# Kernel optimization log

Measured on AMD Instinct MI355X. Metric: run time of the kernel, lower is better.

## Reference

```python
import jax, jax.numpy as jnp
import numpy as np

HIDDEN = 1152
PATCH = 16
POS_SIZE = 64
B = 16
NP_ = 4096
IN_DIM = 3 * PATCH * PATCH  # 768


def setup_inputs() -> dict:
    key = jax.random.key(0)
    k1, k2, k3, k4, k5 = jax.random.split(key, 5)
    pixel_values = jax.random.normal(k1, (B, NP_, IN_DIM), dtype=jnp.float32)
    pixel_position_ids = jax.random.randint(k2, (B, NP_, 2), 0, POS_SIZE, dtype=jnp.int64)
    padding_positions = jax.random.randint(k3, (B, NP_), 0, 2) > 0
    # learned params: nn.Linear(input_dim, hidden, bias=False) weight is [hidden, in_dim]
    W = jax.random.normal(k4, (HIDDEN, IN_DIM), dtype=jnp.float32) / np.sqrt(IN_DIM)
    table = jax.random.normal(k5, (2, POS_SIZE, HIDDEN), dtype=jnp.float32)
    return {
        "pixel_values": pixel_values,
        "pixel_position_ids": pixel_position_ids,
        "padding_positions": padding_positions,
        "W": W,
        "table": table,
    }


def reference(pixel_values, pixel_position_ids, padding_positions, W, table):
    # input_proj: [B, N, in_dim] @ W.T -> [B, N, hidden]
    hidden_states = jnp.einsum("bnd,hd->bnh", pixel_values, W)
    # one_hot + matmul + sum over axis-of-2 is exactly a gather of the x-row
    # from table[0] plus the y-row from table[1]
    pos = jnp.clip(pixel_position_ids, 0, None)  # [B, N, 2]
    pe = table[0][pos[..., 0]] + table[1][pos[..., 1]]  # [B, N, hidden]
    pe = jnp.where(padding_positions[..., None], jnp.zeros_like(pe), pe)
    return hidden_states + pe
```

## Files before the change

### kernel.cpp

```cpp
#include <hip/hip_runtime.h>

#define HIDDEN 1152
#define IN_DIM 768
#define POS_SIZE 64
#define M_TOTAL (16 * 4096)

#define BM 64
#define NPASS 9
#define NSTAGE 12
#define TOTSTAGE (NPASS * NSTAGE)

typedef _Float16 f16x8 __attribute__((ext_vector_type(8)));
typedef float f32x4 __attribute__((ext_vector_type(4)));
typedef float f32x8v __attribute__((ext_vector_type(8)));

typedef __attribute__((address_space(1))) const void global_cv;
typedef __attribute__((address_space(3))) void lds_v;

__device__ __forceinline__ void async16(const void* g, void* l) {
    __builtin_amdgcn_global_load_lds((global_cv*)g, (lds_v*)l, 16, 0, 0);
}

__global__ __launch_bounds__(256) void pack_w(const float* __restrict__ W,
                                              _Float16* __restrict__ Wp) {
    unsigned tid = blockIdx.x * 256 + threadIdx.x;
    unsigned n = tid / 96u;
    unsigned kc = tid - n * 96u;
    f32x8v x = *(const f32x8v*)(W + (size_t)n * IN_DIM + kc * 8u);
    f16x8 h = __builtin_convertvector(x, f16x8);
    unsigned c = (n >> 4) * 1536u + kc * 16u + (n & 15u);
    ((f16x8*)Wp)[c] = h;
}

__global__ __launch_bounds__(512, 2) void gemm_pe(
    const float* __restrict__ A,
    const _Float16* __restrict__ Wp,
    const int* __restrict__ pos,
    const int* __restrict__ pad,
    const float* __restrict__ table,
    float* __restrict__ out) {
    __shared__ __align__(16) _Float16 sA[6144 * 8];
    __shared__ __align__(16) _Float16 sB[8 * 3 * 1024];

    const int m0 = blockIdx.x * BM;
    const int t = threadIdx.x;
    const int lane = t & 63;
    const int w = t >> 6;
    const int quad = lane >> 4;
    const int l15 = lane & 15;

    const f16x8* wp = (const f16x8*)Wp;
    _Float16* myB = &sB[w * 3072];

#pragma unroll
    for (int g = 0; g < 2; ++g)
#pragma unroll
        for (int kk = 0; kk < 2; ++kk)
            async16(wp + (size_t)(w * 1536 + (2 * g + kk) * 64 + lane),
                    myB + (g * 1024 + kk * 512));

    int meta[16];
#pragma unroll
    for (int mi = 0; mi < 4; mi++)
#pragma unroll
        for (int r = 0; r < 4; r++) {
            const int gm = m0 + mi * 16 + quad * 4 + r;
            int px = pos[gm * 2];
            int py = pos[gm * 2 + 1];
            px = px < 0 ? 0 : px;
            py = py < 0 ? 0 : py;
            meta[mi * 4 + r] = px | (py << 8) | ((pad[gm] ? 1 : 0) << 16);
        }

    {
        const float* gA = A + (size_t)m0 * IN_DIM;
#pragma unroll 4
        for (int i = 0; i < 12; i++) {
            int c = t + i * 512;
            int row = c / 96;
            int kc = c - row * 96;
            f32x8v x = *(const f32x8v*)(gA + (size_t)row * IN_DIM + kc * 8);
            f16x8 h = __builtin_convertvector(x, f16x8);
            int chunk = kc * 64 + (row ^ ((kc & 7) << 1));
            *(f16x8*)&sA[(size_t)chunk * 8] = h;
        }
    }
    __syncthreads();

    for (int pass = 0; pass < NPASS; pass++) {
        f32x4 acc[4];
#pragma unroll
        for (int mi = 0; mi < 4; mi++) acc[mi] = (f32x4)0.f;

        for (int s = 0; s < NSTAGE; s++) {
            const int g = pass * NSTAGE + s;
            if (g < TOTSTAGE - 2) {
                const int g2 = g + 2;
                const int p2 = g2 / NSTAGE;
                const int s2 = g2 - p2 * NSTAGE;
                const int slot2 = g2 - (g2 / 3) * 3;
#pragma unroll
                for (int kk = 0; kk < 2; ++kk)
                    async16(wp + (size_t)(p2 * 12288 + w * 1536 + (2 * s2 + kk) * 64 + lane),
                            myB + (slot2 * 1024 + kk * 512));
                asm volatile("s_waitcnt vmcnt(4)" ::: "memory");
            } else if (g == TOTSTAGE - 2) {
                asm volatile("s_waitcnt vmcnt(2)" ::: "memory");
            } else {
                asm volatile("s_waitcnt vmcnt(0)" ::: "memory");
            }

            const int slot = g - (g / 3) * 3;
            f16x8 bf[2];
#pragma unroll
            for (int kk = 0; kk < 2; ++kk)
                bf[kk] = *(const f16x8*)&myB[slot * 1024 + kk * 512 + lane * 8];

            f16x8 af[4][2];
#pragma unroll
            for (int mi = 0; mi < 4; mi++)
#pragma unroll
                for (int kk = 0; kk < 2; kk++) {
                    const int kc = (2 * s + kk) * 4 + quad;
                    const int row = (l15 + mi * 16) ^ ((kc & 7) << 1);
                    af[mi][kk] = *(const f16x8*)&sA[(size_t)(kc * 64 + row) * 8];
                }

            __builtin_amdgcn_s_setprio(1);
#pragma unroll
            for (int kk = 0; kk < 2; kk++)
#pragma unroll
                for (int mi = 0; mi < 4; mi++)
                    acc[mi] = __builtin_amdgcn_mfma_f32_16x16x32_f16(af[mi][kk], bf[kk],
                                                                     acc[mi], 0, 0, 0);
            __builtin_amdgcn_s_setprio(0);
        }

        const int gn = pass * 128 + w * 16 + l15;
#pragma unroll
        for (int mi = 0; mi < 4; mi++)
#pragma unroll
            for (int r = 0; r < 4; r++) {
                const int gm = m0 + mi * 16 + quad * 4 + r;
                const int mv = meta[mi * 4 + r];
                const int px = mv & 255;
                const int py = (mv >> 8) & 255;
                const int isPad = mv >> 16;
                float pe = isPad ? 0.f
                                 : (table[(size_t)px * HIDDEN + gn] +
                                    table[(size_t)(POS_SIZE + py) * HIDDEN + gn]);
                out[(size_t)gm * HIDDEN + gn] = acc[mi][r] + pe;
            }
    }
}

__global__ __launch_bounds__(256) void fallback_naive(const float* __restrict__ A,
                                                      const float* __restrict__ W,
                                                      const int* __restrict__ pos,
                                                      const int* __restrict__ pad,
                                                      const float* __restrict__ table,
                                                      float* __restrict__ out) {
    long idx = (long)blockIdx.x * 256 + threadIdx.x;
    const long total = (long)M_TOTAL * HIDDEN;
    if (idx >= total) return;
    int m = (int)(idx / HIDDEN);
    int n = (int)(idx - (long)m * HIDDEN);
    const float* a = A + (size_t)m * IN_DIM;
    const float* wv = W + (size_t)n * IN_DIM;
    float s = 0.f;
    for (int k = 0; k < IN_DIM; k++) s += a[k] * wv[k];
    int px = pos[m * 2]; if (px < 0) px = 0;
    int py = pos[m * 2 + 1]; if (py < 0) py = 0;
    float pe = pad[m] ? 0.f : (table[(size_t)px * HIDDEN + n] +
                               table[(size_t)(POS_SIZE + py) * HIDDEN + n]);
    out[idx] = s + pe;
}

extern "C" void kernel_launch(void* const* d_in, const int* in_sizes, int n_in,
                              void* d_out, int out_size, void* d_ws, size_t ws_size,
                              hipStream_t stream) {
    const float* pixel = (const float*)d_in[0];
    const int* pos = (const int*)d_in[1];
    const int* pad = (const int*)d_in[2];
    const float* W = (const float*)d_in[3];
    const float* table = (const float*)d_in[4];
    float* out = (float*)d_out;

    const size_t nW = (size_t)HIDDEN * IN_DIM;
    if (ws_size >= nW * sizeof(_Float16)) {
        _Float16* Wp = (_Float16*)d_ws;
        pack_w<<<432, 256, 0, stream>>>(W, Wp);
        gemm_pe<<<M_TOTAL / BM, 512, 0, stream>>>(pixel, Wp, pos, pad, table, out);
    } else {
        long total = (long)M_TOTAL * HIDDEN;
        fallback_naive<<<(int)((total + 255) / 256), 256, 0, stream>>>(pixel, W, pos, pad,
                                                                       table, out);
    }
}
```

Measured before the change: 597.6 us.

## Widen per-wave N tile to 48 columns and reuse A fragments across three MFMAs

Each wave now computes three 16-column output tiles per pass (48 columns, 3 passes instead of 9), so each A fragment read from LDS feeds three MFMAs instead of one. This cuts LDS A-read traffic and pass/epilogue overhead. The W pipeline changes from a 3-slot ring with K=64 per stage to a 2-slot double buffer with K=32 per stage, with an explicit lgkmcnt wait before each async refill. The cost is more accumulator registers and a shallower prefetch depth.

```diff
diff --git a/kernel.cpp b/kernel.cpp
--- a/kernel.cpp
+++ b/kernel.cpp
@@ -6,8 +6,8 @@
 #define M_TOTAL (16 * 4096)
 
 #define BM 64
-#define NPASS 9
-#define NSTAGE 12
+#define NPASS 3
+#define NSTAGE 24
 #define TOTSTAGE (NPASS * NSTAGE)
 
 typedef _Float16 f16x8 __attribute__((ext_vector_type(8)));
@@ -40,7 +40,7 @@
     const float* __restrict__ table,
     float* __restrict__ out) {
     __shared__ __align__(16) _Float16 sA[6144 * 8];
-    __shared__ __align__(16) _Float16 sB[8 * 3 * 1024];
+    __shared__ __align__(16) _Float16 sB[8 * 2 * 1536];
 
     const int m0 = blockIdx.x * BM;
     const int t = threadIdx.x;
@@ -55,9 +55,9 @@
 #pragma unroll
     for (int g = 0; g < 2; ++g)
 #pragma unroll
-        for (int kk = 0; kk < 2; ++kk)
-            async16(wp + (size_t)(w * 1536 + (2 * g + kk) * 64 + lane),
-                    myB + (g * 1024 + kk * 512));
+        for (int j = 0; j < 3; ++j)
+            async16(wp + (size_t)((w * 3 + j) * 1536 + g * 64 + lane),
+                    myB + g * 1536 + j * 512);
 
     int meta[16];
 #pragma unroll
@@ -88,55 +88,56 @@
     __syncthreads();
 
     for (int pass = 0; pass < NPASS; pass++) {
-        f32x4 acc[4];
-#pragma unroll
-        for (int mi = 0; mi < 4; mi++) acc[mi] = (f32x4)0.f;
+        f32x4 acc[4][3];
+#pragma unroll
+        for (int mi = 0; mi < 4; mi++)
+#pragma unroll
+            for (int j = 0; j < 3; j++) acc[mi][j] = (f32x4)0.f;
 
         for (int s = 0; s < NSTAGE; s++) {
             const int g = pass * NSTAGE + s;
+            if (g < TOTSTAGE - 1) {
+                asm volatile("s_waitcnt vmcnt(3)" ::: "memory");
+            } else {
+                asm volatile("s_waitcnt vmcnt(0)" ::: "memory");
+            }
+
+            const int slot = g & 1;
+            f16x8 bf[3];
+#pragma unroll
+            for (int j = 0; j < 3; ++j)
+                bf[j] = *(const f16x8*)&myB[slot * 1536 + j * 512 + lane * 8];
+
+            f16x8 af[4];
+#pragma unroll
+            for (int mi = 0; mi < 4; mi++) {
+                const int kc = s * 4 + quad;
+                const int row = (l15 + mi * 16) ^ ((kc & 7) << 1);
+                af[mi] = *(const f16x8*)&sA[(size_t)(kc * 64 + row) * 8];
+            }
+
+            asm volatile("s_waitcnt lgkmcnt(0)" ::: "memory");
             if (g < TOTSTAGE - 2) {
                 const int g2 = g + 2;
                 const int p2 = g2 / NSTAGE;
                 const int s2 = g2 - p2 * NSTAGE;
-                const int slot2 = g2 - (g2 / 3) * 3;
-#pragma unroll
-                for (int kk = 0; kk < 2; ++kk)
-                    async16(wp + (size_t)(p2 * 12288 + w * 1536 + (2 * s2 + kk) * 64 + lane),
-                            myB + (slot2 * 1024 + kk * 512));
-                asm volatile("s_waitcnt vmcnt(4)" ::: "memory");
-            } else if (g == TOTSTAGE - 2) {
-                asm volatile("s_waitcnt vmcnt(2)" ::: "memory");
-            } else {
-                asm volatile("s_waitcnt vmcnt(0)" ::: "memory");
-            }
-
-            const int slot = g - (g / 3) * 3;
-            f16x8 bf[2];
-#pragma unroll
-            for (int kk = 0; kk < 2; ++kk)
-                bf[kk] = *(const f16x8*)&myB[slot * 1024 + kk * 512 + lane * 8];
-
-            f16x8 af[4][2];
+                const int slot2 = g2 & 1;
+#pragma unroll
+                for (int j = 0; j < 3; ++j)
+                    async16(wp + (size_t)((p2 * 24 + w * 3 + j) * 1536 + s2 * 64 + lane),
+                            myB + slot2 * 1536 + j * 512);
+            }
+
+            __builtin_amdgcn_s_setprio(1);
 #pragma unroll
             for (int mi = 0; mi < 4; mi++)
 #pragma unroll
-                for (int kk = 0; kk < 2; kk++) {
-                    const int kc = (2 * s + kk) * 4 + quad;
-                    const int row = (l15 + mi * 16) ^ ((kc & 7) << 1);
-                    af[mi][kk] = *(const f16x8*)&sA[(size_t)(kc * 64 + row) * 8];
-                }
-
-            __builtin_amdgcn_s_setprio(1);
-#pragma unroll
-            for (int kk = 0; kk < 2; kk++)
-#pragma unroll
-                for (int mi = 0; mi < 4; mi++)
-                    acc[mi] = __builtin_amdgcn_mfma_f32_16x16x32_f16(af[mi][kk], bf[kk],
-                                                                     acc[mi], 0, 0, 0);
+                for (int j = 0; j < 3; j++)
+                    acc[mi][j] = __builtin_amdgcn_mfma_f32_16x16x32_f16(af[mi], bf[j],
+                                                                        acc[mi][j], 0, 0, 0);
             __builtin_amdgcn_s_setprio(0);
         }
 
-        const int gn = pass * 128 + w * 16 + l15;
 #pragma unroll
         for (int mi = 0; mi < 4; mi++)
 #pragma unroll
@@ -146,10 +147,15 @@
                 const int px = mv & 255;
                 const int py = (mv >> 8) & 255;
                 const int isPad = mv >> 16;
-                float pe = isPad ? 0.f
-                                 : (table[(size_t)px * HIDDEN + gn] +
-                                    table[(size_t)(POS_SIZE + py) * HIDDEN + gn]);
-                out[(size_t)gm * HIDDEN + gn] = acc[mi][r] + pe;
+                float* orow = out + (size_t)gm * HIDDEN;
+#pragma unroll
+                for (int j = 0; j < 3; j++) {
+                    const int gn = pass * 384 + w * 48 + j * 16 + l15;
+                    float pe = isPad ? 0.f
+                                     : (table[(size_t)px * HIDDEN + gn] +
+                                        table[(size_t)(POS_SIZE + py) * HIDDEN + gn]);
+                    orow[gn] = acc[mi][j][r] + pe;
+                }
             }
     }
 }
```

Measured after the change: 564.1 us. 5.6% less time.
